# Performance work log

Measured on AMD Instinct MI355X. Metric: run time of the kernel, lower is better.

Reference implementation:

```python
import jax, jax.numpy as jnp
import numpy as np
from jax import lax

IN_DIM, OUT_DIM, GROUPS, K, DEGREE, PAD = 64, 128, 4, 3, 3, 1
IN_G = IN_DIM // GROUPS    # 16
OUT_G = OUT_DIM // GROUPS  # 32
EPS = 1e-5


def setup_inputs() -> dict:
    key = jax.random.key(0)
    k1, k2 = jax.random.split(key)
    x = jax.random.normal(k1, (64, IN_DIM, 64, 64), jnp.float32)
    # meta (hypernetwork-generated) weight: (out_g, in_g*(degree+2), k, k)
    layer_weight = jax.random.normal(k2, (OUT_G, IN_G * (DEGREE + 2), K, K), jnp.float32) * 0.05
    return {"x": x, "layer_weight": layer_weight}


def _conv(x, w):
    # plain NCHW conv2d, groups=1, stride=1, dilation=1, symmetric padding
    return lax.conv_general_dilated(
        x, w, window_strides=(1, 1), padding=[(PAD, PAD), (PAD, PAD)],
        dimension_numbers=("NCHW", "OIHW", "NCHW"))


def _legendre_basis(x, order):
    # recursive Legendre polynomials P0..P_order, concatenated on channel dim
    polys = [jnp.ones_like(x), x]
    for n in range(1, order):
        pn = ((2.0 * n + 1.0) * x * polys[-1] - n * polys[-2]) / (n + 1.0)
        polys.append(pn)
    return jnp.concatenate(polys, axis=1)  # [B, in_g*(order+1), H, W]


def _group_forward(xg, w):
    # xg: [B, in_g, H, W]; w: [out_g, in_g*(degree+2), k, k]
    base_w = w[:, :IN_G]                                   # (out_g, in_g, k, k)
    base_out = _conv(jax.nn.silu(xg), base_w)
    # global min-max normalization over the whole group tensor
    xmin, xmax = xg.min(), xg.max()
    x_norm = 2.0 * (xg - xmin) / (xmax - xmin) - 1.0
    lb = _legendre_basis(x_norm, DEGREE)                   # [B, in_g*(degree+1), H, W]
    poly_w = w[:, IN_G:].reshape(OUT_G, IN_G * (DEGREE + 1), K, K)
    y = base_out + _conv(lb, poly_w)
    # InstanceNorm2d (affine=False, no running stats): per-sample per-channel
    mean = y.mean(axis=(2, 3), keepdims=True)
    var = y.var(axis=(2, 3), keepdims=True)
    y = (y - mean) * lax.rsqrt(var + EPS)
    return jax.nn.silu(y)


def reference(x, layer_weight):
    B, C, H, W = x.shape
    # split channels into groups, vmap over groups (same weight for each group)
    xg = x.reshape(B, GROUPS, IN_G, H, W).transpose(1, 0, 2, 3, 4)  # [G,B,in_g,H,W]
    yg = jax.vmap(lambda xx: _group_forward(xx, layer_weight))(xg)  # [G,B,out_g,H,W]
    return yg.transpose(1, 0, 2, 3, 4).reshape(B, OUT_DIM, H, W)
```

## Files before the change

### kernel.cpp

```cpp
#include <hip/hip_runtime.h>
#include <hip/hip_bf16.h>


#define NB 64
#define NH 64
#define NW 64

typedef __attribute__((ext_vector_type(8)))  short bf16x8;
typedef __attribute__((ext_vector_type(8)))  unsigned short u16x8;
typedef __attribute__((ext_vector_type(16))) float f32x16;

__device__ __forceinline__ float silu(float v) {
    return v / (1.0f + __expf(-v));
}
__device__ __forceinline__ unsigned short tobf(float f) {
    union { __hip_bfloat16 h; unsigned short u; } cv;
    cv.h = __float2bfloat16(f);
    return cv.u;
}

__global__ __launch_bounds__(256) void minmax_kernel(const float* __restrict__ x,
                                                     float* __restrict__ pmm) {
    int plane = blockIdx.x;
    const float4* p = (const float4*)(x + (size_t)plane * 4096);
    int t = threadIdx.x;
    float mn = 3.4e38f, mx = -3.4e38f;
    #pragma unroll
    for (int k = 0; k < 4; ++k) {
        float4 v = p[t + k * 256];
        mn = fminf(mn, fminf(fminf(v.x, v.y), fminf(v.z, v.w)));
        mx = fmaxf(mx, fmaxf(fmaxf(v.x, v.y), fmaxf(v.z, v.w)));
    }
    #pragma unroll
    for (int off = 32; off; off >>= 1) {
        mn = fminf(mn, __shfl_xor(mn, off));
        mx = fmaxf(mx, __shfl_xor(mx, off));
    }
    __shared__ float smn[4], smx[4];
    int wid = t >> 6, lane = t & 63;
    if (lane == 0) { smn[wid] = mn; smx[wid] = mx; }
    __syncthreads();
    if (t == 0) {
        mn = fminf(fminf(smn[0], smn[1]), fminf(smn[2], smn[3]));
        mx = fmaxf(fmaxf(smx[0], smx[1]), fmaxf(smx[2], smx[3]));
        pmm[plane * 2]     = mn;
        pmm[plane * 2 + 1] = mx;
    }
}

__global__ __launch_bounds__(256) void reduce_repack_kernel(const float* __restrict__ pmm,
                                                            const float* __restrict__ w,
                                                            float* __restrict__ wsf,
                                                            unsigned short* __restrict__ wpk,
                                                            float* __restrict__ Tt) {
    int blk = blockIdx.x;
    int t = threadIdx.x;
    if (blk < 4) {
        int g = blk;
        float mn = 3.4e38f, mx = -3.4e38f;
        #pragma unroll
        for (int j = 0; j < 4; ++j) {
            int p = t + j * 256;
            int b = p >> 4, c = p & 15;
            int plane = b * 64 + g * 16 + c;
            mn = fminf(mn, pmm[plane * 2]);
            mx = fmaxf(mx, pmm[plane * 2 + 1]);
        }
        #pragma unroll
        for (int off = 32; off; off >>= 1) {
            mn = fminf(mn, __shfl_xor(mn, off));
            mx = fmaxf(mx, __shfl_xor(mx, off));
        }
        __shared__ float smn[4], smx[4];
        int wid = t >> 6, lane = t & 63;
        if (lane == 0) { smn[wid] = mn; smx[wid] = mx; }
        __syncthreads();
        if (t == 0) {
            mn = fminf(fminf(smn[0], smn[1]), fminf(smn[2], smn[3]));
            mx = fmaxf(fmaxf(smx[0], smx[1]), fmaxf(smx[2], smx[3]));
            wsf[g * 2]     = mn;
            wsf[g * 2 + 1] = mx;
        }
    } else if (blk < 76) {
        int idx = (blk - 4) * 256 + t;
        int p   = idx / 4608;
        int r1  = idx - p * 4608;
        int tap = r1 / 512;
        int r2  = r1 - tap * 512;
        int h   = r2 >> 8;
        int oc  = (r2 >> 3) & 31;
        int j   = r2 & 7;
        int k   = p * 16 + h * 8 + j;
        int orig = (k < 16) ? k : (k + 16);
        wpk[idx] = tobf(w[oc * 720 + orig * 9 + tap]);
    } else {
        for (int i = t; i < 288; i += 256) {
            int oc = i / 9, ty = i - oc * 9;
            int ey = ty / 3, ex = ty - ey * 3;
            int ky0 = (ey == 0) ? 1 : 0, ky1 = (ey == 2) ? 1 : 2;
            int kx0 = (ex == 0) ? 1 : 0, kx1 = (ex == 2) ? 1 : 2;
            float s = 0.f;
            for (int c = 0; c < 16; ++c)
                for (int ky = ky0; ky <= ky1; ++ky)
                    for (int kx = kx0; kx <= kx1; ++kx)
                        s += w[oc * 720 + (16 + c) * 9 + ky * 3 + kx];
            Tt[i] = s;
        }
    }
}

__global__ __launch_bounds__(512, 6) void conv_mfma_kernel(const float* __restrict__ x,
                                                           const float* __restrict__ wsf,
                                                           const unsigned short* __restrict__ wpk,
                                                           const float* __restrict__ Tt,
                                                           float* __restrict__ out,
                                                           unsigned short* __restrict__ yscr) {
    __shared__ unsigned short wl[18432];
    __shared__ unsigned short augp[5184];
    __shared__ float Tl[288];

    int flat = blockIdx.x;
    int f = ((flat & 7) << 9) | (flat >> 3);
    int tile = f & 15;
    int bg = f >> 4;
    int b = bg & 63;
    int g = bg >> 6;
    int th0 = (tile >> 2) * 16, tw0 = (tile & 3) * 16;

    float xmin = wsf[g * 2];
    float xmax = wsf[g * 2 + 1];
    float inv = 2.0f / (xmax - xmin);

    const float* xg = x + ((size_t)b * 64 + g * 16) * 4096;
    int t = threadIdx.x;

    {
        const uint4* srcw = (const uint4*)wpk;
        uint4* dstw = (uint4*)wl;
        #pragma unroll
        for (int i = 0; i < 5; ++i) {
            int idx = t + i * 512;
            if (idx < 2304) dstw[idx] = srcw[idx];
        }
    }
    if (t < 288) Tl[t] = Tt[t];

    float r[2][8];
    bool okv[2];
    #pragma unroll
    for (int i = 0; i < 2; ++i) {
        okv[i] = false;
        int idx = t + i * 512;
        if (idx < 648) {
            int half = idx >= 324 ? 1 : 0;
            int pix = idx - half * 324;
            int ly = pix / 18, lx = pix - ly * 18;
            int gh = th0 + ly - 1, gw = tw0 + lx - 1;
            bool ok = (gh >= 0 && gh < NH && gw >= 0 && gw < NW);
            okv[i] = ok;
            const float* s = xg + (size_t)(half * 8) * 4096 + gh * 64 + gw;
            #pragma unroll
            for (int j = 0; j < 8; ++j)
                r[i][j] = ok ? s[(size_t)j * 4096] : 0.f;
        }
    }

    int wv = t >> 6;
    int lane = t & 63;
    int lo = lane & 31, hi = lane >> 5;
    int py = 2 * wv + (lo >> 4), px = lo & 15;

    f32x16 acc = {};

    #pragma unroll
    for (int p = 0; p < 4; ++p) {
        #pragma unroll
        for (int i = 0; i < 2; ++i) {
            int idx = t + i * 512;
            if (idx < 648) {
                int half = idx >= 324 ? 1 : 0;
                int pix = idx - half * 324;
                bf16x8 v;
                #pragma unroll
                for (int j = 0; j < 8; ++j) {
                    float val = r[i][j];
                    float o;
                    if (p == 0) {
                        o = silu(val);
                    } else {
                        float xn = (val - xmin) * inv - 1.f;
                        if (p == 1) o = xn;
                        else {
                            float x2 = xn * xn;
                            o = (p == 2) ? (1.5f * x2 - 0.5f) : ((2.5f * x2 - 1.5f) * xn);
                        }
                        o = okv[i] ? o : 0.f;
                    }
                    v[j] = (short)tobf(o);
                }
                *(bf16x8*)&augp[(half * 324 + pix) * 8] = v;
            }
        }
        __syncthreads();

        #pragma unroll
        for (int tap = 0; tap < 9; ++tap) {
            const int ky = tap / 3, kx = tap % 3;
            const int hp = (py + ky) * 18 + (px + kx);
            bf16x8 Af = *(const bf16x8*)&wl[(((p * 9 + tap) * 2 + hi) * 32 + lo) * 8];
            bf16x8 Bf = *(const bf16x8*)&augp[(hi * 324 + hp) * 8];
            acc = __builtin_amdgcn_mfma_f32_32x32x16_bf16(Af, Bf, acc, 0, 0, 0);
        }
        __syncthreads();
    }

    int h = th0 + py, wc = tw0 + px;
    int ey = (h == 0) ? 0 : ((h == NH - 1) ? 2 : 1);
    int ex = (wc == 0) ? 0 : ((wc == NW - 1) ? 2 : 1);
    int et = ey * 3 + ex;
    size_t obase = ((size_t)b * 128 + g * 32) * 4096 + (size_t)h * 64 + wc;
    if (yscr) {
        #pragma unroll
        for (int rr = 0; rr < 16; ++rr) {
            int oc = (rr & 3) + 8 * (rr >> 2) + 4 * hi;
            yscr[obase + (size_t)oc * 4096] = tobf(acc[rr] + Tl[oc * 9 + et]);
        }
    } else {
        #pragma unroll
        for (int rr = 0; rr < 16; ++rr) {
            int oc = (rr & 3) + 8 * (rr >> 2) + 4 * hi;
            out[obase + (size_t)oc * 4096] = acc[rr] + Tl[oc * 9 + et];
        }
    }
}

__global__ __launch_bounds__(256) void norm_bf16_kernel(const unsigned short* __restrict__ yscr,
                                                        float* __restrict__ out) {
    int plane = blockIdx.x;
    const u16x8* p = (const u16x8*)(yscr + (size_t)plane * 4096);
    int t = threadIdx.x;
    float v[2][8];
    float s = 0.f, s2 = 0.f;
    #pragma unroll
    for (int k = 0; k < 2; ++k) {
        u16x8 u = p[t + k * 256];
        #pragma unroll
        for (int j = 0; j < 8; ++j) {
            float f = __uint_as_float((unsigned)u[j] << 16);
            v[k][j] = f;
            s += f;
            s2 += f * f;
        }
    }
    #pragma unroll
    for (int off = 32; off; off >>= 1) {
        s  += __shfl_xor(s, off);
        s2 += __shfl_xor(s2, off);
    }
    __shared__ float ss[4], ss2[4];
    int wid = t >> 6, lane = t & 63;
    if (lane == 0) { ss[wid] = s; ss2[wid] = s2; }
    __syncthreads();
    s  = ss[0] + ss[1] + ss[2] + ss[3];
    s2 = ss2[0] + ss2[1] + ss2[2] + ss2[3];
    float mean = s * (1.f / 4096.f);
    float var  = fmaxf(s2 * (1.f / 4096.f) - mean * mean, 0.f);
    float istd = rsqrtf(var + 1e-5f);
    float4* o = (float4*)(out + (size_t)plane * 4096);
    #pragma unroll
    for (int k = 0; k < 2; ++k) {
        float4 a, bq;
        a.x = silu((v[k][0] - mean) * istd);
        a.y = silu((v[k][1] - mean) * istd);
        a.z = silu((v[k][2] - mean) * istd);
        a.w = silu((v[k][3] - mean) * istd);
        bq.x = silu((v[k][4] - mean) * istd);
        bq.y = silu((v[k][5] - mean) * istd);
        bq.z = silu((v[k][6] - mean) * istd);
        bq.w = silu((v[k][7] - mean) * istd);
        o[(t + k * 256) * 2]     = a;
        o[(t + k * 256) * 2 + 1] = bq;
    }
}

__global__ __launch_bounds__(256) void norm_kernel(float* __restrict__ out) {
    int plane = blockIdx.x;
    float4* p = (float4*)(out + (size_t)plane * 4096);
    int t = threadIdx.x;
    float4 v[4];
    float s = 0.f, s2 = 0.f;
    #pragma unroll
    for (int k = 0; k < 4; ++k) {
        v[k] = p[t + k * 256];
        s  += v[k].x + v[k].y + v[k].z + v[k].w;
        s2 += v[k].x * v[k].x + v[k].y * v[k].y + v[k].z * v[k].z + v[k].w * v[k].w;
    }
    #pragma unroll
    for (int off = 32; off; off >>= 1) {
        s  += __shfl_xor(s, off);
        s2 += __shfl_xor(s2, off);
    }
    __shared__ float ss[4], ss2[4];
    int wid = t >> 6, lane = t & 63;
    if (lane == 0) { ss[wid] = s; ss2[wid] = s2; }
    __syncthreads();
    s  = ss[0] + ss[1] + ss[2] + ss[3];
    s2 = ss2[0] + ss2[1] + ss2[2] + ss2[3];
    float mean = s * (1.f / 4096.f);
    float var  = fmaxf(s2 * (1.f / 4096.f) - mean * mean, 0.f);
    float istd = rsqrtf(var + 1e-5f);
    #pragma unroll
    for (int k = 0; k < 4; ++k) {
        float4 o;
        o.x = (v[k].x - mean) * istd; o.x = silu(o.x);
        o.y = (v[k].y - mean) * istd; o.y = silu(o.y);
        o.z = (v[k].z - mean) * istd; o.z = silu(o.z);
        o.w = (v[k].w - mean) * istd; o.w = silu(o.w);
        p[t + k * 256] = o;
    }
}

extern "C" void kernel_launch(void* const* d_in, const int* in_sizes, int n_in,
                              void* d_out, int out_size, void* d_ws, size_t ws_size,
                              hipStream_t stream) {
    const float* x = (const float*)d_in[0];
    const float* w = (const float*)d_in[1];
    float* out = (float*)d_out;
    float* wsf = (float*)d_ws;
    float* pmm = (float*)((char*)d_ws + 64);
    unsigned short* wpk = (unsigned short*)((char*)d_ws + 64 + 32768);
    float* Tt = (float*)((char*)d_ws + 64 + 32768 + 36864);

    const size_t YSCR_OFF = 131072;
    const size_t YSCR_BYTES = (size_t)64 * 128 * 4096 * 2;
    unsigned short* yscr = (ws_size >= YSCR_OFF + YSCR_BYTES)
                         ? (unsigned short*)((char*)d_ws + YSCR_OFF) : nullptr;

    hipLaunchKernelGGL(minmax_kernel, dim3(NB * 64), dim3(256), 0, stream, x, pmm);
    hipLaunchKernelGGL(reduce_repack_kernel, dim3(77), dim3(256), 0, stream, pmm, w, wsf, wpk, Tt);
    hipLaunchKernelGGL(conv_mfma_kernel, dim3(4096), dim3(512), 0, stream, x, wsf, wpk, Tt, out, yscr);
    if (yscr)
        hipLaunchKernelGGL(norm_bf16_kernel, dim3(NB * 128), dim3(256), 0, stream, yscr, out);
    else
        hipLaunchKernelGGL(norm_kernel, dim3(NB * 128), dim3(256), 0, stream, out);
}
```

Measured before the change: 132.4 us.

## Double-buffer LDS basis tiles and load MFMA weights directly into registers

Drops the shared-memory copy of the packed weights and instead has each lane load its MFMA A-fragments straight from global memory into registers, prefetching the next polynomial stage's weights while the current stage runs. The basis/silu staging tile is double-buffered in LDS so computing stage p+1 overlaps the MFMAs of stage p, which removes one barrier per stage. The launch-bounds occupancy hint drops from 6 to 4 waves to make room for the extra register pressure of holding two weight sets. The risks are lower occupancy and repeated global/L2 weight reads in every block.

```diff
diff --git a/kernel.cpp b/kernel.cpp
--- a/kernel.cpp
+++ b/kernel.cpp
@@ -109,14 +109,13 @@
     }
 }
 
-__global__ __launch_bounds__(512, 6) void conv_mfma_kernel(const float* __restrict__ x,
+__global__ __launch_bounds__(512, 4) void conv_mfma_kernel(const float* __restrict__ x,
                                                            const float* __restrict__ wsf,
                                                            const unsigned short* __restrict__ wpk,
                                                            const float* __restrict__ Tt,
                                                            float* __restrict__ out,
                                                            unsigned short* __restrict__ yscr) {
-    __shared__ unsigned short wl[18432];
-    __shared__ unsigned short augp[5184];
+    __shared__ unsigned short aug2[2][5184];
     __shared__ float Tl[288];
 
     int flat = blockIdx.x;
@@ -133,17 +132,18 @@
 
     const float* xg = x + ((size_t)b * 64 + g * 16) * 4096;
     int t = threadIdx.x;
-
-    {
-        const uint4* srcw = (const uint4*)wpk;
-        uint4* dstw = (uint4*)wl;
-        #pragma unroll
-        for (int i = 0; i < 5; ++i) {
-            int idx = t + i * 512;
-            if (idx < 2304) dstw[idx] = srcw[idx];
-        }
-    }
     if (t < 288) Tl[t] = Tt[t];
+
+    int wv = t >> 6;
+    int lane = t & 63;
+    int lo = lane & 31, hi = lane >> 5;
+    int py = 2 * wv + (lo >> 4), px = lo & 15;
+
+    const bf16x8* wp = (const bf16x8*)wpk;
+    bf16x8 W[2][9];
+    #pragma unroll
+    for (int tap = 0; tap < 9; ++tap)
+        W[0][tap] = wp[(tap * 2 + hi) * 32 + lo];
 
     float r[2][8];
     bool okv[2];
@@ -165,15 +165,7 @@
         }
     }
 
-    int wv = t >> 6;
-    int lane = t & 63;
-    int lo = lane & 31, hi = lane >> 5;
-    int py = 2 * wv + (lo >> 4), px = lo & 15;
-
-    f32x16 acc = {};
-
-    #pragma unroll
-    for (int p = 0; p < 4; ++p) {
+    auto stage = [&](int p, unsigned short* buf) {
         #pragma unroll
         for (int i = 0; i < 2; ++i) {
             int idx = t + i * 512;
@@ -198,18 +190,38 @@
                     }
                     v[j] = (short)tobf(o);
                 }
-                *(bf16x8*)&augp[(half * 324 + pix) * 8] = v;
+                *(bf16x8*)&buf[(half * 324 + pix) * 8] = v;
             }
         }
-        __syncthreads();
+    };
+
+    stage(0, aug2[0]);
+    __syncthreads();
+
+    f32x16 acc = {};
+
+    #pragma unroll
+    for (int p = 0; p < 4; ++p) {
+        const int cb = p & 1, nb = cb ^ 1;
+        if (p < 3) {
+            #pragma unroll
+            for (int tap = 0; tap < 9; ++tap)
+                W[nb][tap] = wp[(((p + 1) * 9 + tap) * 2 + hi) * 32 + lo];
+            stage(p + 1, aug2[nb]);
+        }
 
         #pragma unroll
         for (int tap = 0; tap < 9; ++tap) {
             const int ky = tap / 3, kx = tap % 3;
             const int hp = (py + ky) * 18 + (px + kx);
-            bf16x8 Af = *(const bf16x8*)&wl[(((p * 9 + tap) * 2 + hi) * 32 + lo) * 8];
-            bf16x8 Bf = *(const bf16x8*)&augp[(hi * 324 + hp) * 8];
-            acc = __builtin_amdgcn_mfma_f32_32x32x16_bf16(Af, Bf, acc, 0, 0, 0);
+            bf16x8 Bf = *(const bf16x8*)&aug2[cb][(hi * 324 + hp) * 8];
+            acc = __builtin_amdgcn_mfma_f32_32x32x16_bf16(W[cb][tap], Bf, acc, 0, 0, 0);
+        }
+
+        if (p < 3) {
+            #pragma unroll
+            for (int tap = 0; tap < 9; ++tap)
+                asm volatile("" : "+v"(W[nb][tap]));
         }
         __syncthreads();
     }
```

New measurement: 162.1 us. 1.22x slower.

## Fold group min-max reduction into conv kernel and process two tiles per block

Applied to the files above, without the earlier changes.

The per-group min/max reduction moves out of the repack kernel and into each conv block, which now reduces the 1024 per-plane partials itself. Each conv block also handles two spatial tiles in sequence, halving the grid to 2048 blocks. This spreads the 36 KB weight staging into LDS and the min-max reduction over twice the work. In exchange every block repeats the redundant partial reduction plus two extra barriers, and the grid now has fewer blocks to fill the GPU.

```diff
diff --git a/kernel.cpp b/kernel.cpp
--- a/kernel.cpp
+++ b/kernel.cpp
@@ -48,41 +48,13 @@
     }
 }
 
-__global__ __launch_bounds__(256) void reduce_repack_kernel(const float* __restrict__ pmm,
-                                                            const float* __restrict__ w,
-                                                            float* __restrict__ wsf,
-                                                            unsigned short* __restrict__ wpk,
-                                                            float* __restrict__ Tt) {
+__global__ __launch_bounds__(256) void repack_kernel(const float* __restrict__ w,
+                                                     unsigned short* __restrict__ wpk,
+                                                     float* __restrict__ Tt) {
     int blk = blockIdx.x;
     int t = threadIdx.x;
-    if (blk < 4) {
-        int g = blk;
-        float mn = 3.4e38f, mx = -3.4e38f;
-        #pragma unroll
-        for (int j = 0; j < 4; ++j) {
-            int p = t + j * 256;
-            int b = p >> 4, c = p & 15;
-            int plane = b * 64 + g * 16 + c;
-            mn = fminf(mn, pmm[plane * 2]);
-            mx = fmaxf(mx, pmm[plane * 2 + 1]);
-        }
-        #pragma unroll
-        for (int off = 32; off; off >>= 1) {
-            mn = fminf(mn, __shfl_xor(mn, off));
-            mx = fmaxf(mx, __shfl_xor(mx, off));
-        }
-        __shared__ float smn[4], smx[4];
-        int wid = t >> 6, lane = t & 63;
-        if (lane == 0) { smn[wid] = mn; smx[wid] = mx; }
-        __syncthreads();
-        if (t == 0) {
-            mn = fminf(fminf(smn[0], smn[1]), fminf(smn[2], smn[3]));
-            mx = fmaxf(fmaxf(smx[0], smx[1]), fmaxf(smx[2], smx[3]));
-            wsf[g * 2]     = mn;
-            wsf[g * 2 + 1] = mx;
-        }
-    } else if (blk < 76) {
-        int idx = (blk - 4) * 256 + t;
+    if (blk < 72) {
+        int idx = blk * 256 + t;
         int p   = idx / 4608;
         int r1  = idx - p * 4608;
         int tap = r1 / 512;
@@ -110,7 +82,7 @@
 }
 
 __global__ __launch_bounds__(512, 6) void conv_mfma_kernel(const float* __restrict__ x,
-                                                           const float* __restrict__ wsf,
+                                                           const float* __restrict__ pmm,
                                                            const unsigned short* __restrict__ wpk,
                                                            const float* __restrict__ Tt,
                                                            float* __restrict__ out,
@@ -118,18 +90,15 @@
     __shared__ unsigned short wl[18432];
     __shared__ unsigned short augp[5184];
     __shared__ float Tl[288];
+    __shared__ float mmbc[2];
+    __shared__ float smn[8], smx[8];
 
     int flat = blockIdx.x;
-    int f = ((flat & 7) << 9) | (flat >> 3);
-    int tile = f & 15;
-    int bg = f >> 4;
+    int f = ((flat & 7) << 8) | (flat >> 3);
+    int tp = f & 7;
+    int bg = f >> 3;
     int b = bg & 63;
     int g = bg >> 6;
-    int th0 = (tile >> 2) * 16, tw0 = (tile & 3) * 16;
-
-    float xmin = wsf[g * 2];
-    float xmax = wsf[g * 2 + 1];
-    float inv = 2.0f / (xmax - xmin);
 
     const float* xg = x + ((size_t)b * 64 + g * 16) * 4096;
     int t = threadIdx.x;
@@ -145,91 +114,130 @@
     }
     if (t < 288) Tl[t] = Tt[t];
 
-    float r[2][8];
-    bool okv[2];
-    #pragma unroll
-    for (int i = 0; i < 2; ++i) {
-        okv[i] = false;
-        int idx = t + i * 512;
-        if (idx < 648) {
-            int half = idx >= 324 ? 1 : 0;
-            int pix = idx - half * 324;
-            int ly = pix / 18, lx = pix - ly * 18;
-            int gh = th0 + ly - 1, gw = tw0 + lx - 1;
-            bool ok = (gh >= 0 && gh < NH && gw >= 0 && gw < NW);
-            okv[i] = ok;
-            const float* s = xg + (size_t)(half * 8) * 4096 + gh * 64 + gw;
-            #pragma unroll
-            for (int j = 0; j < 8; ++j)
-                r[i][j] = ok ? s[(size_t)j * 4096] : 0.f;
-        }
-    }
+    {
+        float mn = 3.4e38f, mx = -3.4e38f;
+        #pragma unroll
+        for (int j = 0; j < 2; ++j) {
+            int p = t + j * 512;
+            int bb = p >> 4, cc = p & 15;
+            int plane = bb * 64 + g * 16 + cc;
+            mn = fminf(mn, pmm[plane * 2]);
+            mx = fmaxf(mx, pmm[plane * 2 + 1]);
+        }
+        #pragma unroll
+        for (int off = 32; off; off >>= 1) {
+            mn = fminf(mn, __shfl_xor(mn, off));
+            mx = fmaxf(mx, __shfl_xor(mx, off));
+        }
+        int wid = t >> 6, lane = t & 63;
+        if (lane == 0) { smn[wid] = mn; smx[wid] = mx; }
+    }
+    __syncthreads();
+    if (t == 0) {
+        float mn = smn[0], mx = smx[0];
+        #pragma unroll
+        for (int i = 1; i < 8; ++i) {
+            mn = fminf(mn, smn[i]);
+            mx = fmaxf(mx, smx[i]);
+        }
+        mmbc[0] = mn;
+        mmbc[1] = mx;
+    }
+    __syncthreads();
+    float xmin = mmbc[0];
+    float inv = 2.0f / (mmbc[1] - xmin);
 
     int wv = t >> 6;
     int lane = t & 63;
     int lo = lane & 31, hi = lane >> 5;
     int py = 2 * wv + (lo >> 4), px = lo & 15;
 
-    f32x16 acc = {};
-
-    #pragma unroll
-    for (int p = 0; p < 4; ++p) {
+    for (int tp2 = 0; tp2 < 2; ++tp2) {
+        int tile = tp * 2 + tp2;
+        int th0 = (tile >> 2) * 16, tw0 = (tile & 3) * 16;
+
+        float r[2][8];
+        bool okv[2];
         #pragma unroll
         for (int i = 0; i < 2; ++i) {
+            okv[i] = false;
             int idx = t + i * 512;
             if (idx < 648) {
                 int half = idx >= 324 ? 1 : 0;
                 int pix = idx - half * 324;
-                bf16x8 v;
+                int ly = pix / 18, lx = pix - ly * 18;
+                int gh = th0 + ly - 1, gw = tw0 + lx - 1;
+                bool ok = (gh >= 0 && gh < NH && gw >= 0 && gw < NW);
+                okv[i] = ok;
+                const float* s = xg + (size_t)(half * 8) * 4096 + gh * 64 + gw;
                 #pragma unroll
-                for (int j = 0; j < 8; ++j) {
-                    float val = r[i][j];
-                    float o;
-                    if (p == 0) {
-                        o = silu(val);
-                    } else {
-                        float xn = (val - xmin) * inv - 1.f;
-                        if (p == 1) o = xn;
-                        else {
-                            float x2 = xn * xn;
-                            o = (p == 2) ? (1.5f * x2 - 0.5f) : ((2.5f * x2 - 1.5f) * xn);
+                for (int j = 0; j < 8; ++j)
+                    r[i][j] = ok ? s[(size_t)j * 4096] : 0.f;
+            }
+        }
+
+        f32x16 acc = {};
+
+        #pragma unroll
+        for (int p = 0; p < 4; ++p) {
+            #pragma unroll
+            for (int i = 0; i < 2; ++i) {
+                int idx = t + i * 512;
+                if (idx < 648) {
+                    int half = idx >= 324 ? 1 : 0;
+                    int pix = idx - half * 324;
+                    bf16x8 v;
+                    #pragma unroll
+                    for (int j = 0; j < 8; ++j) {
+                        float val = r[i][j];
+                        float o;
+                        if (p == 0) {
+                            o = silu(val);
+                        } else {
+                            float xn = (val - xmin) * inv - 1.f;
+                            if (p == 1) o = xn;
+                            else {
+                                float x2 = xn * xn;
+                                o = (p == 2) ? (1.5f * x2 - 0.5f)
+                                             : ((2.5f * x2 - 1.5f) * xn);
+                            }
+                            o = okv[i] ? o : 0.f;
                         }
-                        o = okv[i] ? o : 0.f;
+                        v[j] = (short)tobf(o);
                     }
-                    v[j] = (short)tobf(o);
+                    *(bf16x8*)&augp[(half * 324 + pix) * 8] = v;
                 }
-                *(bf16x8*)&augp[(half * 324 + pix) * 8] = v;
-            }
-        }
-        __syncthreads();
-
-        #pragma unroll
-        for (int tap = 0; tap < 9; ++tap) {
-            const int ky = tap / 3, kx = tap % 3;
-            const int hp = (py + ky) * 18 + (px + kx);
-            bf16x8 Af = *(const bf16x8*)&wl[(((p * 9 + tap) * 2 + hi) * 32 + lo) * 8];
-            bf16x8 Bf = *(const bf16x8*)&augp[(hi * 324 + hp) * 8];
-            acc = __builtin_amdgcn_mfma_f32_32x32x16_bf16(Af, Bf, acc, 0, 0, 0);
-        }
-        __syncthreads();
-    }
-
-    int h = th0 + py, wc = tw0 + px;
-    int ey = (h == 0) ? 0 : ((h == NH - 1) ? 2 : 1);
-    int ex = (wc == 0) ? 0 : ((wc == NW - 1) ? 2 : 1);
-    int et = ey * 3 + ex;
-    size_t obase = ((size_t)b * 128 + g * 32) * 4096 + (size_t)h * 64 + wc;
-    if (yscr) {
-        #pragma unroll
-        for (int rr = 0; rr < 16; ++rr) {
-            int oc = (rr & 3) + 8 * (rr >> 2) + 4 * hi;
-            yscr[obase + (size_t)oc * 4096] = tobf(acc[rr] + Tl[oc * 9 + et]);
-        }
-    } else {
-        #pragma unroll
-        for (int rr = 0; rr < 16; ++rr) {
-            int oc = (rr & 3) + 8 * (rr >> 2) + 4 * hi;
-            out[obase + (size_t)oc * 4096] = acc[rr] + Tl[oc * 9 + et];
+            }
+            __syncthreads();
+
+            #pragma unroll
+            for (int tap = 0; tap < 9; ++tap) {
+                const int ky = tap / 3, kx = tap % 3;
+                const int hp = (py + ky) * 18 + (px + kx);
+                bf16x8 Af = *(const bf16x8*)&wl[(((p * 9 + tap) * 2 + hi) * 32 + lo) * 8];
+                bf16x8 Bf = *(const bf16x8*)&augp[(hi * 324 + hp) * 8];
+                acc = __builtin_amdgcn_mfma_f32_32x32x16_bf16(Af, Bf, acc, 0, 0, 0);
+            }
+            __syncthreads();
+        }
+
+        int h = th0 + py, wc = tw0 + px;
+        int ey = (h == 0) ? 0 : ((h == NH - 1) ? 2 : 1);
+        int ex = (wc == 0) ? 0 : ((wc == NW - 1) ? 2 : 1);
+        int et = ey * 3 + ex;
+        size_t obase = ((size_t)b * 128 + g * 32) * 4096 + (size_t)h * 64 + wc;
+        if (yscr) {
+            #pragma unroll
+            for (int rr = 0; rr < 16; ++rr) {
+                int oc = (rr & 3) + 8 * (rr >> 2) + 4 * hi;
+                yscr[obase + (size_t)oc * 4096] = tobf(acc[rr] + Tl[oc * 9 + et]);
+            }
+        } else {
+            #pragma unroll
+            for (int rr = 0; rr < 16; ++rr) {
+                int oc = (rr & 3) + 8 * (rr >> 2) + 4 * hi;
+                out[obase + (size_t)oc * 4096] = acc[rr] + Tl[oc * 9 + et];
+            }
         }
     }
 }
@@ -326,7 +334,6 @@
     const float* x = (const float*)d_in[0];
     const float* w = (const float*)d_in[1];
     float* out = (float*)d_out;
-    float* wsf = (float*)d_ws;
     float* pmm = (float*)((char*)d_ws + 64);
     unsigned short* wpk = (unsigned short*)((char*)d_ws + 64 + 32768);
     float* Tt = (float*)((char*)d_ws + 64 + 32768 + 36864);
@@ -337,8 +344,8 @@
                          ? (unsigned short*)((char*)d_ws + YSCR_OFF) : nullptr;
 
     hipLaunchKernelGGL(minmax_kernel, dim3(NB * 64), dim3(256), 0, stream, x, pmm);
-    hipLaunchKernelGGL(reduce_repack_kernel, dim3(77), dim3(256), 0, stream, pmm, w, wsf, wpk, Tt);
-    hipLaunchKernelGGL(conv_mfma_kernel, dim3(4096), dim3(512), 0, stream, x, wsf, wpk, Tt, out, yscr);
+    hipLaunchKernelGGL(repack_kernel, dim3(73), dim3(256), 0, stream, w, wpk, Tt);
+    hipLaunchKernelGGL(conv_mfma_kernel, dim3(2048), dim3(512), 0, stream, x, pmm, wpk, Tt, out, yscr);
     if (yscr)
         hipLaunchKernelGGL(norm_bf16_kernel, dim3(NB * 128), dim3(256), 0, stream, yscr, out);
     else
```

New measurement: 294.1 us. 122% more time.
